# Performance work log

Hardware: AMD Instinct MI355X
Metric: run time of the kernel (lower is better)

The kernel has to match this reference:

```python
import jax, jax.numpy as jnp
import numpy as np

B, S, D, H = 2, 2048, 1024, 16
HD = D // H  # head dim = 64


def setup_inputs() -> dict:
    key = jax.random.key(0)
    ks = jax.random.split(key, 12)
    s = 1.0 / np.sqrt(D)
    return {
        "query": jax.random.normal(ks[0], (B, S, D), jnp.float32),
        "key": jax.random.normal(ks[1], (B, S, D), jnp.float32),
        "value": jax.random.normal(ks[2], (B, S, D), jnp.float32),
        "mask": jax.random.randint(ks[3], (B, S, S), 0, 2, jnp.int32),
        "wq_kernel": jax.random.normal(ks[4], (D, D), jnp.float32) * s,
        "wq_bias": jnp.zeros((D,), jnp.float32),
        "wk_kernel": jax.random.normal(ks[5], (D, D), jnp.float32) * s,
        "wk_bias": jnp.zeros((D,), jnp.float32),
        "wv_kernel": jax.random.normal(ks[6], (D, D), jnp.float32) * s,
        "wv_bias": jnp.zeros((D,), jnp.float32),
        "wo_kernel": jax.random.normal(ks[7], (D, D), jnp.float32) * s,
        "wo_bias": jnp.zeros((D,), jnp.float32),
    }


def reference(query, key, value, mask,
              wq_kernel, wq_bias, wk_kernel, wk_bias,
              wv_kernel, wv_bias, wo_kernel, wo_bias):
    b = query.shape[0]
    # Dense projections, then split heads: [B,S,D] -> [B,H,S,HD]
    def split_heads(x):
        return x.reshape(b, -1, H, HD).transpose(0, 2, 1, 3)

    q = split_heads(query @ wq_kernel + wq_bias)
    k = split_heads(key @ wk_kernel + wk_bias)
    v = split_heads(value @ wv_kernel + wv_bias)

    scores = jnp.einsum('bhqd,bhkd->bhqk', q, k) / jnp.sqrt(jnp.float32(HD))
    m = mask[:, None, :, :]  # [B,1,S,S] broadcast over heads
    scores = jnp.where(m == 0, jnp.float32(-1e9), scores)
    attn = jax.nn.softmax(scores, axis=-1)
    out = jnp.einsum('bhqk,bhkd->bhqd', attn, v)
    out = out.transpose(0, 2, 1, 3).reshape(b, -1, D)  # [B,S,D]
    return out @ wo_kernel + wo_bias
```

## Files before the change

### kernel.cpp

```cpp
#include <hip/hip_runtime.h>
#include <hip/hip_bf16.h>

typedef __attribute__((ext_vector_type(8))) short bf16x8;
typedef __attribute__((ext_vector_type(4))) float f32x4;
typedef __attribute__((ext_vector_type(2))) unsigned int u32x2;
typedef unsigned long long u64;
typedef unsigned short u16;
typedef unsigned int u32;

#define LOG2E 1.44269504088896340736f

__device__ __forceinline__ u16 f2bf(float f) {
  u32 u = __builtin_bit_cast(u32, f);
  u32 r = u + 0x7FFFu + ((u >> 16) & 1u);
  return (u16)(r >> 16);
}

__device__ __forceinline__ u32 cvt_pk_bf16(float lo, float hi) {
  u32 r;
  asm("v_cvt_pk_bf16_f32 %0, %1, %2" : "=v"(r) : "v"(lo), "v"(hi));
  return r;
}

__device__ __forceinline__ float fexp2(float x) {
#if __has_builtin(__builtin_amdgcn_exp2f)
  return __builtin_amdgcn_exp2f(x);
#else
  return exp2f(x);
#endif
}

__device__ __forceinline__ void gload16(const u16* g, u16* l) {
  __builtin_amdgcn_global_load_lds(
      (const __attribute__((address_space(1))) u32*)g,
      (__attribute__((address_space(3))) u32*)l, 16, 0, 0);
}

__global__ __launch_bounds__(256) void cvt_bf16(const float* __restrict__ q,
                                                const float* __restrict__ k,
                                                const float* __restrict__ v,
                                                u16* __restrict__ out) {
  const float* src = (blockIdx.y == 0) ? q : (blockIdx.y == 1) ? k : v;
  u16* dst = out + (size_t)blockIdx.y * 4194304;
  size_t i = ((size_t)blockIdx.x * 256 + threadIdx.x) * 8;
  float4 a = *(const float4*)(src + i);
  float4 b = *(const float4*)(src + i + 4);
  u16 t[8] = {f2bf(a.x), f2bf(a.y), f2bf(a.z), f2bf(a.w),
              f2bf(b.x), f2bf(b.y), f2bf(b.z), f2bf(b.w)};
  *(bf16x8*)(dst + i) = *(bf16x8*)t;
}

__global__ __launch_bounds__(256) void mask_bits(const int* __restrict__ mask,
                                                 u64* __restrict__ out) {
  const int nwords = 2 * 2048 * 32;
  int gw = (blockIdx.x * 256 + threadIdx.x) >> 6;
  int lane = threadIdx.x & 63;
  int nw = (gridDim.x * 256) >> 6;
  for (int w = gw; w < nwords; w += nw) {
    int m = mask[(size_t)w * 64 + lane];
    u64 bits = __ballot(m != 0);
    if (lane == 0) out[w] = bits;
  }
}

__global__ __launch_bounds__(256) void wtrans(const float* __restrict__ W0,
                                              const float* __restrict__ W1,
                                              const float* __restrict__ W2,
                                              const float* __restrict__ W3,
                                              u16* __restrict__ WtBase) {
  const float* W = (blockIdx.z == 0) ? W0 : (blockIdx.z == 1) ? W1
                    : (blockIdx.z == 2) ? W2 : W3;
  u16* T = WtBase + (size_t)blockIdx.z * 1048576;
  __shared__ float tile[32][33];
  int k0 = blockIdx.y * 32, n0 = blockIdx.x * 32;
  int tx = threadIdx.x, ty = threadIdx.y;
#pragma unroll
  for (int i = 0; i < 4; i++)
    tile[ty + i * 8][tx] = W[(size_t)(k0 + ty + i * 8) * 1024 + n0 + tx];
  __syncthreads();
#pragma unroll
  for (int i = 0; i < 4; i++)
    T[(size_t)(n0 + ty + i * 8) * 1024 + k0 + tx] = f2bf(tile[tx][ty + i * 8]);
}

__global__ __launch_bounds__(256) void vtrans(const u16* __restrict__ Vb,
                                              u16* __restrict__ Vt) {
  __shared__ u16 t[64][72];
  int bh = blockIdx.y, k0 = blockIdx.x * 64;
  const u16* src = Vb + (size_t)bh * 2048 * 64;
  u16* dst = Vt + (size_t)bh * 64 * 2048;
  int tid = threadIdx.x;
  int r = tid >> 2, c = (tid & 3) * 16;
  *(bf16x8*)&t[r][c] = *(const bf16x8*)(src + (size_t)(k0 + r) * 64 + c);
  *(bf16x8*)&t[r][c + 8] = *(const bf16x8*)(src + (size_t)(k0 + r) * 64 + c + 8);
  __syncthreads();
  int d = tid >> 2, kb = (tid & 3) * 16;
  u16 tmp[16];
#pragma unroll
  for (int i = 0; i < 16; i++) tmp[i] = t[kb + i][d];
  *(bf16x8*)(dst + (size_t)d * 2048 + k0 + kb) = *(bf16x8*)&tmp[0];
  *(bf16x8*)(dst + (size_t)d * 2048 + k0 + kb + 8) = *(bf16x8*)&tmp[8];
}

__global__ __launch_bounds__(256, 2) void gemm_qkv(
    const u16* __restrict__ Ab, const float* __restrict__ bq,
    const float* __restrict__ bk, const float* __restrict__ bv,
    const u16* __restrict__ WtBase, u16* __restrict__ OutBase) {
  constexpr int K = 1024;
  __shared__ alignas(16) u16 As[128][32];
  __shared__ alignas(16) u16 Bs[128][32];
  const int z = blockIdx.z;
  const u16* A = Ab + (size_t)z * 4194304;
  const float* bias = (z == 0) ? bq : (z == 1) ? bk : bv;
  const u16* Bt = WtBase + (size_t)z * 1048576;
  u16* Ob = OutBase + (size_t)z * 4194304;
  const float scale = (z == 0) ? 0.125f * LOG2E : 1.0f;

  const int tid = threadIdx.x;
  const int lane = tid & 63, wave = tid >> 6;
  const int wr = wave >> 1, wc = wave & 1;
  const int m0 = blockIdx.y * 128, n0 = blockIdx.x * 128;
  const int fr = lane & 15, fq = lane >> 4;

  const int srow = lane >> 2, scol = (lane & 3) * 8;
  const u16* Agp = A + (size_t)(m0 + wave * 32 + srow) * K + scol;
  const u16* Bgp = Bt + (size_t)(n0 + wave * 32 + srow) * K + scol;
  u16* As0 = &As[wave * 32][0];
  u16* As1 = &As[wave * 32 + 16][0];
  u16* Bs0 = &Bs[wave * 32][0];
  u16* Bs1 = &Bs[wave * 32 + 16][0];

  f32x4 acc[4][4];
#pragma unroll
  for (int i = 0; i < 4; i++)
#pragma unroll
    for (int j = 0; j < 4; j++) acc[i][j] = (f32x4){0.f, 0.f, 0.f, 0.f};

  for (int k0 = 0; k0 < K; k0 += 32) {
    gload16(Agp + k0, As0);
    gload16(Agp + k0 + 16 * K, As1);
    gload16(Bgp + k0, Bs0);
    gload16(Bgp + k0 + 16 * K, Bs1);
    __syncthreads();
    bf16x8 af[4], bfv[4];
#pragma unroll
    for (int i = 0; i < 4; i++) {
      af[i] = *(const bf16x8*)&As[wr * 64 + i * 16 + fr][fq * 8];
      bfv[i] = *(const bf16x8*)&Bs[wc * 64 + i * 16 + fr][fq * 8];
    }
#pragma unroll
    for (int i = 0; i < 4; i++)
#pragma unroll
      for (int j = 0; j < 4; j++)
        acc[i][j] = __builtin_amdgcn_mfma_f32_16x16x32_bf16(af[i], bfv[j],
                                                            acc[i][j], 0, 0, 0);
    __syncthreads();
  }
#pragma unroll
  for (int j = 0; j < 4; j++) {
    int col = n0 + wc * 64 + j * 16 + fr;
    float bcol = bias[col];
    int hh = col >> 6, hd = col & 63;
#pragma unroll
    for (int i = 0; i < 4; i++) {
#pragma unroll
      for (int r = 0; r < 4; r++) {
        int row = m0 + wr * 64 + i * 16 + fq * 4 + r;
        int bb = row >> 11, ss = row & 2047;
        float val = (acc[i][j][r] + bcol) * scale;
        Ob[(((size_t)bb * 16 + hh) * 2048 + ss) * 64 + hd] = f2bf(val);
      }
    }
  }
}

__global__ __launch_bounds__(256, 2) void gemm_out(const u16* __restrict__ A,
                                                   const u16* __restrict__ Bt,
                                                   const float* __restrict__ bias,
                                                   float* __restrict__ Out) {
  constexpr int K = 1024;
  __shared__ alignas(16) u16 As[64][32];
  __shared__ alignas(16) u16 Bs[128][32];
  const int tid = threadIdx.x;
  const int lane = tid & 63, wave = tid >> 6;
  const int wr = wave >> 1, wc = wave & 1;
  const int m0 = blockIdx.y * 64, n0 = blockIdx.x * 128;
  const int fr = lane & 15, fq = lane >> 4;

  const int srow = lane >> 2, scol = (lane & 3) * 8;
  const u16* Agp = A + (size_t)(m0 + wave * 16 + srow) * K + scol;
  const u16* Bgp = Bt + (size_t)(n0 + wave * 32 + srow) * K + scol;
  u16* As0 = &As[wave * 16][0];
  u16* Bs0 = &Bs[wave * 32][0];
  u16* Bs1 = &Bs[wave * 32 + 16][0];

  f32x4 acc[2][4];
#pragma unroll
  for (int i = 0; i < 2; i++)
#pragma unroll
    for (int j = 0; j < 4; j++) acc[i][j] = (f32x4){0.f, 0.f, 0.f, 0.f};

  for (int k0 = 0; k0 < K; k0 += 32) {
    gload16(Agp + k0, As0);
    gload16(Bgp + k0, Bs0);
    gload16(Bgp + k0 + 16 * K, Bs1);
    __syncthreads();
    bf16x8 af[2], bfv[4];
#pragma unroll
    for (int i = 0; i < 2; i++)
      af[i] = *(const bf16x8*)&As[wr * 32 + i * 16 + fr][fq * 8];
#pragma unroll
    for (int j = 0; j < 4; j++)
      bfv[j] = *(const bf16x8*)&Bs[wc * 64 + j * 16 + fr][fq * 8];
#pragma unroll
    for (int i = 0; i < 2; i++)
#pragma unroll
      for (int j = 0; j < 4; j++)
        acc[i][j] = __builtin_amdgcn_mfma_f32_16x16x32_bf16(af[i], bfv[j],
                                                            acc[i][j], 0, 0, 0);
    __syncthreads();
  }
#pragma unroll
  for (int j = 0; j < 4; j++) {
    int col = n0 + wc * 64 + j * 16 + fr;
    float bcol = bias[col];
#pragma unroll
    for (int i = 0; i < 2; i++) {
#pragma unroll
      for (int r = 0; r < 4; r++) {
        int row = m0 + wr * 32 + i * 16 + fq * 4 + r;
        Out[(size_t)row * 1024 + col] = acc[i][j][r] + bcol;
      }
    }
  }
}

__global__ __launch_bounds__(256, 4) void attn(const u16* __restrict__ Qb,
                                               const u16* __restrict__ Kb,
                                               const u16* __restrict__ Vtb,
                                               const u64* __restrict__ mbits,
                                               u16* __restrict__ AO) {
  int fid = blockIdx.x + (blockIdx.y << 5) + ((int)blockIdx.z << 9);
  int nfid = ((fid & 7) << 7) + (fid >> 3);
  const int qt = nfid & 31, h = (nfid >> 5) & 15, b = nfid >> 9;
  const int bh = b * 16 + h, q0 = qt * 64;
  const u16* Qh = Qb + (size_t)bh * 2048 * 64;
  const u16* Kh = Kb + (size_t)bh * 2048 * 64;
  const u16* Vh = Vtb + (size_t)bh * 64 * 2048;

  __shared__ u16 Kbuf[2][64][64];
  __shared__ u16 Vbuf[2][64][64];
  __shared__ u16 Ps[4][16][64];

  const int tid = threadIdx.x, lane = tid & 63, wave = tid >> 6;
  const int fr = lane & 15, fq = lane >> 4;
  const int l3 = lane >> 3, l7 = lane & 7;
  const int srcoff = ((l7 ^ l3) * 8);
  const int sw = fr & 7;
  const int sw4 = sw << 4;

  {
    const u16* qsrc = Qh + (size_t)(q0 + wave * 16 + l3) * 64 + srcoff;
    gload16(qsrc, &Vbuf[1][wave * 16][0]);
    gload16(qsrc + 8 * 64, &Vbuf[1][wave * 16 + 8][0]);
    const u16* ksrc = Kh + (size_t)(wave * 16 + l3) * 64 + srcoff;
    gload16(ksrc, &Kbuf[0][wave * 16][0]);
    gload16(ksrc + 8 * 64, &Kbuf[0][wave * 16 + 8][0]);
    const u16* vsrc = Vh + (size_t)(wave * 16 + l3) * 2048 + srcoff;
    gload16(vsrc, &Vbuf[0][wave * 16][0]);
    gload16(vsrc + 8 * 2048, &Vbuf[0][wave * 16 + 8][0]);
  }
  __syncthreads();
  bf16x8 qf0 = *(const bf16x8*)&Vbuf[1][wave * 16 + fr][(fq ^ sw) * 8];
  bf16x8 qf1 = *(const bf16x8*)&Vbuf[1][wave * 16 + fr][((4 + fq) ^ sw) * 8];
  __syncthreads();

  f32x4 accO[4];
#pragma unroll
  for (int i = 0; i < 4; i++) accO[i] = (f32x4){0.f, 0.f, 0.f, 0.f};
  float mrun = -1e30f, lrun = 0.f;

  const u64* mrow = mbits + ((size_t)b * 2048 + q0 + wave * 16 + fr) * 32;
  const u16* kpre = Kh + (size_t)(64 + wave * 16 + l3) * 64 + srcoff;
  const u16* vpre = Vh + (size_t)(wave * 16 + l3) * 2048 + 64 + srcoff;
  u64 wcur = mrow[0];

  for (int kt = 0; kt < 32; kt++) {
    const int cur = kt & 1, nxt = cur ^ 1;
    u64 wnxt = 0;
    if (kt < 31) {
      gload16(kpre, &Kbuf[nxt][wave * 16][0]);
      gload16(kpre + 8 * 64, &Kbuf[nxt][wave * 16 + 8][0]);
      gload16(vpre, &Vbuf[nxt][wave * 16][0]);
      gload16(vpre + 8 * 2048, &Vbuf[nxt][wave * 16 + 8][0]);
      kpre += 64 * 64;
      vpre += 64;
      wnxt = mrow[kt + 1];
    }
    u32 wlo = (u32)wcur, whi = (u32)(wcur >> 32);

    f32x4 sf[4];
    __builtin_amdgcn_s_setprio(1);
#pragma unroll
    for (int f = 0; f < 4; f++) {
      u32 half = (f & 2) ? whi : wlo;
      u32 nib = (half >> ((f & 1) * 16 + fq * 4)) & 0xFu;
      f32x4 zz;
      zz[0] = (nib & 1u) ? 0.f : -3e38f;
      zz[1] = (nib & 2u) ? 0.f : -3e38f;
      zz[2] = (nib & 4u) ? 0.f : -3e38f;
      zz[3] = (nib & 8u) ? 0.f : -3e38f;
      bf16x8 kf0 = *(const bf16x8*)&Kbuf[cur][f * 16 + fr][(fq ^ sw) * 8];
      bf16x8 kf1 = *(const bf16x8*)&Kbuf[cur][f * 16 + fr][((4 + fq) ^ sw) * 8];
      zz = __builtin_amdgcn_mfma_f32_16x16x32_bf16(kf0, qf0, zz, 0, 0, 0);
      zz = __builtin_amdgcn_mfma_f32_16x16x32_bf16(kf1, qf1, zz, 0, 0, 0);
      sf[f] = zz;
    }
    __builtin_amdgcn_s_setprio(0);

    float t0 = fmaxf(fmaxf(sf[0][0], sf[0][1]), sf[0][2]);
    float t1 = fmaxf(fmaxf(sf[0][3], sf[1][0]), sf[1][1]);
    float t2 = fmaxf(fmaxf(sf[1][2], sf[1][3]), sf[2][0]);
    float t3 = fmaxf(fmaxf(sf[2][1], sf[2][2]), sf[2][3]);
    float t4 = fmaxf(fmaxf(sf[3][0], sf[3][1]), sf[3][2]);
    float rm = fmaxf(fmaxf(fmaxf(t0, t1), fmaxf(t2, t3)),
                     fmaxf(t4, sf[3][3]));
    rm = fmaxf(rm, __shfl_xor(rm, 16));
    rm = fmaxf(rm, __shfl_xor(rm, 32));
    if (!__all(rm <= mrun + 8.f)) {
      float mnew = fmaxf(mrun, rm);
      float sc = fexp2(mrun - mnew);
      mrun = mnew;
      lrun *= sc;
      float sc0 = __shfl(sc, fq * 4 + 0);
      float sc1 = __shfl(sc, fq * 4 + 1);
      float sc2 = __shfl(sc, fq * 4 + 2);
      float sc3 = __shfl(sc, fq * 4 + 3);
#pragma unroll
      for (int hs = 0; hs < 4; hs++) {
        accO[hs][0] *= sc0;
        accO[hs][1] *= sc1;
        accO[hs][2] *= sc2;
        accO[hs][3] *= sc3;
      }
    }
    float rs = 0.f;
    u32 pk0[4], pk1[4];
#pragma unroll
    for (int f = 0; f < 4; f++) {
      float p0 = fexp2(sf[f][0] - mrun);
      float p1 = fexp2(sf[f][1] - mrun);
      float p2 = fexp2(sf[f][2] - mrun);
      float p3 = fexp2(sf[f][3] - mrun);
      rs += (p0 + p1) + (p2 + p3);
      pk0[f] = cvt_pk_bf16(p0, p1);
      pk1[f] = cvt_pk_bf16(p2, p3);
    }
    rs += __shfl_xor(rs, 16);
    rs += __shfl_xor(rs, 32);
    lrun += rs;
    char* Pw = (char*)&Ps[wave][fr][0];
#pragma unroll
    for (int f = 0; f < 4; f++) {
      int boff = (f * 32 + fq * 8) ^ sw4;
      *(u32x2*)(Pw + boff) = (u32x2){pk0[f], pk1[f]};
    }
    __builtin_amdgcn_s_setprio(1);
#pragma unroll
    for (int ks = 0; ks < 2; ks++) {
      bf16x8 pa = *(const bf16x8*)(Pw + (((ks * 4 + fq) << 4) ^ sw4));
#pragma unroll
      for (int hs = 0; hs < 4; hs++) {
        bf16x8 vf =
            *(const bf16x8*)&Vbuf[cur][hs * 16 + fr][((ks * 4 + fq) ^ sw) * 8];
        accO[hs] =
            __builtin_amdgcn_mfma_f32_16x16x32_bf16(pa, vf, accO[hs], 0, 0, 0);
      }
    }
    __builtin_amdgcn_s_setprio(0);
    wcur = wnxt;
    __syncthreads();
  }
  float lq0 = fmaxf(__shfl(lrun, fq * 4 + 0), 1e-30f);
  float lq1 = fmaxf(__shfl(lrun, fq * 4 + 1), 1e-30f);
  float lq2 = fmaxf(__shfl(lrun, fq * 4 + 2), 1e-30f);
  float lq3 = fmaxf(__shfl(lrun, fq * 4 + 3), 1e-30f);
#pragma unroll
  for (int hs = 0; hs < 4; hs++) {
    int d = hs * 16 + fr;
    size_t base = ((size_t)b * 2048 + q0 + wave * 16) * 1024 + h * 64 + d;
    AO[base + (size_t)(fq * 4 + 0) * 1024] = f2bf(accO[hs][0] / lq0);
    AO[base + (size_t)(fq * 4 + 1) * 1024] = f2bf(accO[hs][1] / lq1);
    AO[base + (size_t)(fq * 4 + 2) * 1024] = f2bf(accO[hs][2] / lq2);
    AO[base + (size_t)(fq * 4 + 3) * 1024] = f2bf(accO[hs][3] / lq3);
  }
}

extern "C" void kernel_launch(void* const* d_in, const int* in_sizes, int n_in,
                              void* d_out, int out_size, void* d_ws,
                              size_t ws_size, hipStream_t stream) {
  const float* q = (const float*)d_in[0];
  const float* k = (const float*)d_in[1];
  const float* v = (const float*)d_in[2];
  const int* mask = (const int*)d_in[3];
  const float* wq = (const float*)d_in[4];
  const float* bq = (const float*)d_in[5];
  const float* wk = (const float*)d_in[6];
  const float* bk = (const float*)d_in[7];
  const float* wv = (const float*)d_in[8];
  const float* bv = (const float*)d_in[9];
  const float* wo = (const float*)d_in[10];
  const float* bo = (const float*)d_in[11];

  char* ws = (char*)d_ws;
  u16* Wt = (u16*)(ws);
  u16* Qb = (u16*)(ws + (size_t)(8u << 20));
  u16* Kb = (u16*)(ws + (size_t)(16u << 20));
  u16* Vb = (u16*)(ws + (size_t)(24u << 20));
  u16* Ab = (u16*)(ws + (size_t)(32u << 20));
  u16* AO = (u16*)(ws + (size_t)(32u << 20));
  u64* mb = (u64*)(ws + (size_t)(40u << 20));
  u16* Vt = (u16*)(ws + (size_t)(41u << 20));

  cvt_bf16<<<dim3(2048, 3), dim3(256), 0, stream>>>(q, k, v, Ab);
  wtrans<<<dim3(32, 32, 4), dim3(32, 8), 0, stream>>>(wq, wk, wv, wo, Wt);
  gemm_qkv<<<dim3(8, 32, 3), dim3(256), 0, stream>>>(Ab, bq, bk, bv, Wt, Qb);
  mask_bits<<<dim3(2048), dim3(256), 0, stream>>>(mask, mb);
  vtrans<<<dim3(32, 32), dim3(256), 0, stream>>>(Vb, Vt);
  attn<<<dim3(32, 16, 2), dim3(256), 0, stream>>>(Qb, Kb, Vt, mb, AO);
  gemm_out<<<dim3(8, 64, 1), dim3(256), 0, stream>>>(AO, Wt + 3 * 1048576, bo,
                                                     (float*)d_out);
}
```

Measured before the change: 159.3 us.

## Rewrite attention with 32x32 MFMA tiles, 128-query blocks and register P

The attention kernel now gives each wave 32 queries instead of 16, so a block covers 128 queries, and it uses 32x32x16 bf16 MFMA for both QK^T and PV. The probability tile is passed from the score accumulators to the PV operand in registers with v_permlane32_swap, so the per-wave LDS round trip for P is gone. Output is staged through LDS so each row is written to global memory with 16-byte stores. This halves K/V reloads per query and cuts shuffles, but it raises register use (launch bounds drop to 2 blocks) and halves the grid to 512 blocks.

```diff
diff --git a/kernel.cpp b/kernel.cpp
--- a/kernel.cpp
+++ b/kernel.cpp
@@ -3,7 +3,9 @@
 
 typedef __attribute__((ext_vector_type(8))) short bf16x8;
 typedef __attribute__((ext_vector_type(4))) float f32x4;
+typedef __attribute__((ext_vector_type(16))) float f32x16;
 typedef __attribute__((ext_vector_type(2))) unsigned int u32x2;
+typedef __attribute__((ext_vector_type(4))) unsigned int u32x4;
 typedef unsigned long long u64;
 typedef unsigned short u16;
 typedef unsigned int u32;
@@ -20,6 +22,10 @@
   u32 r;
   asm("v_cvt_pk_bf16_f32 %0, %1, %2" : "=v"(r) : "v"(lo), "v"(hi));
   return r;
+}
+
+__device__ __forceinline__ void swap32(u32& a, u32& b) {
+  asm("v_permlane32_swap_b32 %0, %1" : "+v"(a), "+v"(b));
 }
 
 __device__ __forceinline__ float fexp2(float x) {
@@ -235,164 +241,188 @@
   }
 }
 
-__global__ __launch_bounds__(256, 4) void attn(const u16* __restrict__ Qb,
+__global__ __launch_bounds__(256, 2) void attn(const u16* __restrict__ Qb,
                                                const u16* __restrict__ Kb,
                                                const u16* __restrict__ Vtb,
                                                const u64* __restrict__ mbits,
                                                u16* __restrict__ AO) {
-  int fid = blockIdx.x + (blockIdx.y << 5) + ((int)blockIdx.z << 9);
-  int nfid = ((fid & 7) << 7) + (fid >> 3);
-  const int qt = nfid & 31, h = (nfid >> 5) & 15, b = nfid >> 9;
-  const int bh = b * 16 + h, q0 = qt * 64;
+  const int fid = blockIdx.x;
+  const int nfid = ((fid & 7) << 6) + (fid >> 3);
+  const int qt = nfid & 15, bh = nfid >> 4;
+  const int h = bh & 15, b = bh >> 4;
+  const int q0 = qt * 128;
   const u16* Qh = Qb + (size_t)bh * 2048 * 64;
   const u16* Kh = Kb + (size_t)bh * 2048 * 64;
   const u16* Vh = Vtb + (size_t)bh * 64 * 2048;
 
-  __shared__ u16 Kbuf[2][64][64];
-  __shared__ u16 Vbuf[2][64][64];
-  __shared__ u16 Ps[4][16][64];
+  __shared__ u16 smem[18432];
+  u16* KB = smem;
+  u16* VB = smem + 8192;
 
   const int tid = threadIdx.x, lane = tid & 63, wave = tid >> 6;
-  const int fr = lane & 15, fq = lane >> 4;
-  const int l3 = lane >> 3, l7 = lane & 7;
-  const int srcoff = ((l7 ^ l3) * 8);
-  const int sw = fr & 7;
-  const int sw4 = sw << 4;
+  const int ql = lane & 31, hi = lane >> 5;
+  const int l3 = (lane >> 3) & 7, l7 = lane & 7;
+  const int srcoff = (l7 ^ l3) * 8;
+  const int swz = ql & 7;
 
   {
-    const u16* qsrc = Qh + (size_t)(q0 + wave * 16 + l3) * 64 + srcoff;
-    gload16(qsrc, &Vbuf[1][wave * 16][0]);
-    gload16(qsrc + 8 * 64, &Vbuf[1][wave * 16 + 8][0]);
     const u16* ksrc = Kh + (size_t)(wave * 16 + l3) * 64 + srcoff;
-    gload16(ksrc, &Kbuf[0][wave * 16][0]);
-    gload16(ksrc + 8 * 64, &Kbuf[0][wave * 16 + 8][0]);
+    gload16(ksrc, KB + wave * 16 * 64);
+    gload16(ksrc + 8 * 64, KB + (wave * 16 + 8) * 64);
     const u16* vsrc = Vh + (size_t)(wave * 16 + l3) * 2048 + srcoff;
-    gload16(vsrc, &Vbuf[0][wave * 16][0]);
-    gload16(vsrc + 8 * 2048, &Vbuf[0][wave * 16 + 8][0]);
-  }
-  __syncthreads();
-  bf16x8 qf0 = *(const bf16x8*)&Vbuf[1][wave * 16 + fr][(fq ^ sw) * 8];
-  bf16x8 qf1 = *(const bf16x8*)&Vbuf[1][wave * 16 + fr][((4 + fq) ^ sw) * 8];
-  __syncthreads();
-
-  f32x4 accO[4];
-#pragma unroll
-  for (int i = 0; i < 4; i++) accO[i] = (f32x4){0.f, 0.f, 0.f, 0.f};
+    gload16(vsrc, VB + wave * 16 * 64);
+    gload16(vsrc + 8 * 2048, VB + (wave * 16 + 8) * 64);
+  }
+  const int q = q0 + wave * 32 + ql;
+  bf16x8 qf[4];
+  {
+    const u16* qp = Qh + (size_t)q * 64 + hi * 8;
+#pragma unroll
+    for (int kd = 0; kd < 4; kd++) qf[kd] = *(const bf16x8*)(qp + kd * 16);
+  }
+  f32x16 accO0, accO1;
+#pragma unroll
+  for (int i = 0; i < 16; i++) {
+    accO0[i] = 0.f;
+    accO1[i] = 0.f;
+  }
   float mrun = -1e30f, lrun = 0.f;
-
-  const u64* mrow = mbits + ((size_t)b * 2048 + q0 + wave * 16 + fr) * 32;
+  const u64* mrow = mbits + ((size_t)b * 2048 + q) * 32;
   const u16* kpre = Kh + (size_t)(64 + wave * 16 + l3) * 64 + srcoff;
   const u16* vpre = Vh + (size_t)(wave * 16 + l3) * 2048 + 64 + srcoff;
   u64 wcur = mrow[0];
+  __syncthreads();
 
   for (int kt = 0; kt < 32; kt++) {
-    const int cur = kt & 1, nxt = cur ^ 1;
+    const int cur = kt & 1;
+    const u16* KBc = KB + cur * 4096;
+    const u16* VBc = VB + cur * 4096;
+    u16* KBn = KB + (cur ^ 1) * 4096;
+    u16* VBn = VB + (cur ^ 1) * 4096;
     u64 wnxt = 0;
     if (kt < 31) {
-      gload16(kpre, &Kbuf[nxt][wave * 16][0]);
-      gload16(kpre + 8 * 64, &Kbuf[nxt][wave * 16 + 8][0]);
-      gload16(vpre, &Vbuf[nxt][wave * 16][0]);
-      gload16(vpre + 8 * 2048, &Vbuf[nxt][wave * 16 + 8][0]);
+      gload16(kpre, KBn + wave * 16 * 64);
+      gload16(kpre + 8 * 64, KBn + (wave * 16 + 8) * 64);
+      gload16(vpre, VBn + wave * 16 * 64);
+      gload16(vpre + 8 * 2048, VBn + (wave * 16 + 8) * 64);
       kpre += 64 * 64;
       vpre += 64;
       wnxt = mrow[kt + 1];
     }
-    u32 wlo = (u32)wcur, whi = (u32)(wcur >> 32);
-
-    f32x4 sf[4];
+    const u32 wlo = (u32)wcur, wh = (u32)(wcur >> 32);
+
+    f32x16 sf0, sf1;
+#pragma unroll
+    for (int g = 0; g < 4; g++) {
+      u32 nib0 = (wlo >> (8 * g + 4 * hi)) & 0xFu;
+      u32 nib1 = (wh >> (8 * g + 4 * hi)) & 0xFu;
+      sf0[4 * g + 0] = (nib0 & 1u) ? 0.f : -3e38f;
+      sf0[4 * g + 1] = (nib0 & 2u) ? 0.f : -3e38f;
+      sf0[4 * g + 2] = (nib0 & 4u) ? 0.f : -3e38f;
+      sf0[4 * g + 3] = (nib0 & 8u) ? 0.f : -3e38f;
+      sf1[4 * g + 0] = (nib1 & 1u) ? 0.f : -3e38f;
+      sf1[4 * g + 1] = (nib1 & 2u) ? 0.f : -3e38f;
+      sf1[4 * g + 2] = (nib1 & 4u) ? 0.f : -3e38f;
+      sf1[4 * g + 3] = (nib1 & 8u) ? 0.f : -3e38f;
+    }
     __builtin_amdgcn_s_setprio(1);
 #pragma unroll
-    for (int f = 0; f < 4; f++) {
-      u32 half = (f & 2) ? whi : wlo;
-      u32 nib = (half >> ((f & 1) * 16 + fq * 4)) & 0xFu;
-      f32x4 zz;
-      zz[0] = (nib & 1u) ? 0.f : -3e38f;
-      zz[1] = (nib & 2u) ? 0.f : -3e38f;
-      zz[2] = (nib & 4u) ? 0.f : -3e38f;
-      zz[3] = (nib & 8u) ? 0.f : -3e38f;
-      bf16x8 kf0 = *(const bf16x8*)&Kbuf[cur][f * 16 + fr][(fq ^ sw) * 8];
-      bf16x8 kf1 = *(const bf16x8*)&Kbuf[cur][f * 16 + fr][((4 + fq) ^ sw) * 8];
-      zz = __builtin_amdgcn_mfma_f32_16x16x32_bf16(kf0, qf0, zz, 0, 0, 0);
-      zz = __builtin_amdgcn_mfma_f32_16x16x32_bf16(kf1, qf1, zz, 0, 0, 0);
-      sf[f] = zz;
+    for (int kd = 0; kd < 4; kd++) {
+      bf16x8 kf0 = *(const bf16x8*)&KBc[ql * 64 + ((2 * kd + hi) ^ swz) * 8];
+      bf16x8 kf1 =
+          *(const bf16x8*)&KBc[(32 + ql) * 64 + ((2 * kd + hi) ^ swz) * 8];
+      sf0 = __builtin_amdgcn_mfma_f32_32x32x16_bf16(kf0, qf[kd], sf0, 0, 0, 0);
+      sf1 = __builtin_amdgcn_mfma_f32_32x32x16_bf16(kf1, qf[kd], sf1, 0, 0, 0);
     }
     __builtin_amdgcn_s_setprio(0);
 
-    float t0 = fmaxf(fmaxf(sf[0][0], sf[0][1]), sf[0][2]);
-    float t1 = fmaxf(fmaxf(sf[0][3], sf[1][0]), sf[1][1]);
-    float t2 = fmaxf(fmaxf(sf[1][2], sf[1][3]), sf[2][0]);
-    float t3 = fmaxf(fmaxf(sf[2][1], sf[2][2]), sf[2][3]);
-    float t4 = fmaxf(fmaxf(sf[3][0], sf[3][1]), sf[3][2]);
-    float rm = fmaxf(fmaxf(fmaxf(t0, t1), fmaxf(t2, t3)),
-                     fmaxf(t4, sf[3][3]));
-    rm = fmaxf(rm, __shfl_xor(rm, 16));
+    float rm = fmaxf(sf0[0], sf0[1]);
+#pragma unroll
+    for (int i = 2; i < 16; i += 2) rm = fmaxf(rm, fmaxf(sf0[i], sf0[i + 1]));
+#pragma unroll
+    for (int i = 0; i < 16; i += 2) rm = fmaxf(rm, fmaxf(sf1[i], sf1[i + 1]));
     rm = fmaxf(rm, __shfl_xor(rm, 32));
     if (!__all(rm <= mrun + 8.f)) {
       float mnew = fmaxf(mrun, rm);
       float sc = fexp2(mrun - mnew);
       mrun = mnew;
       lrun *= sc;
-      float sc0 = __shfl(sc, fq * 4 + 0);
-      float sc1 = __shfl(sc, fq * 4 + 1);
-      float sc2 = __shfl(sc, fq * 4 + 2);
-      float sc3 = __shfl(sc, fq * 4 + 3);
-#pragma unroll
-      for (int hs = 0; hs < 4; hs++) {
-        accO[hs][0] *= sc0;
-        accO[hs][1] *= sc1;
-        accO[hs][2] *= sc2;
-        accO[hs][3] *= sc3;
+#pragma unroll
+      for (int i = 0; i < 16; i++) {
+        accO0[i] *= sc;
+        accO1[i] *= sc;
       }
     }
     float rs = 0.f;
-    u32 pk0[4], pk1[4];
-#pragma unroll
-    for (int f = 0; f < 4; f++) {
-      float p0 = fexp2(sf[f][0] - mrun);
-      float p1 = fexp2(sf[f][1] - mrun);
-      float p2 = fexp2(sf[f][2] - mrun);
-      float p3 = fexp2(sf[f][3] - mrun);
-      rs += (p0 + p1) + (p2 + p3);
-      pk0[f] = cvt_pk_bf16(p0, p1);
-      pk1[f] = cvt_pk_bf16(p2, p3);
-    }
-    rs += __shfl_xor(rs, 16);
+#pragma unroll
+    for (int i = 0; i < 16; i++) {
+      sf0[i] = fexp2(sf0[i] - mrun);
+      rs += sf0[i];
+    }
+#pragma unroll
+    for (int i = 0; i < 16; i++) {
+      sf1[i] = fexp2(sf1[i] - mrun);
+      rs += sf1[i];
+    }
     rs += __shfl_xor(rs, 32);
     lrun += rs;
-    char* Pw = (char*)&Ps[wave][fr][0];
-#pragma unroll
-    for (int f = 0; f < 4; f++) {
-      int boff = (f * 32 + fq * 8) ^ sw4;
-      *(u32x2*)(Pw + boff) = (u32x2){pk0[f], pk1[f]};
-    }
+
+    bf16x8 pf[4];
+#pragma unroll
+    for (int g = 0; g < 4; g++) {
+      int r0 = (g & 1) * 8;
+      u32 A, A2, Bv, B2;
+      if (g < 2) {
+        A = cvt_pk_bf16(sf0[r0 + 0], sf0[r0 + 1]);
+        A2 = cvt_pk_bf16(sf0[r0 + 2], sf0[r0 + 3]);
+        Bv = cvt_pk_bf16(sf0[r0 + 4], sf0[r0 + 5]);
+        B2 = cvt_pk_bf16(sf0[r0 + 6], sf0[r0 + 7]);
+      } else {
+        A = cvt_pk_bf16(sf1[r0 + 0], sf1[r0 + 1]);
+        A2 = cvt_pk_bf16(sf1[r0 + 2], sf1[r0 + 3]);
+        Bv = cvt_pk_bf16(sf1[r0 + 4], sf1[r0 + 5]);
+        B2 = cvt_pk_bf16(sf1[r0 + 6], sf1[r0 + 7]);
+      }
+      swap32(A, Bv);
+      swap32(A2, B2);
+      u32x4 t = (u32x4){A, A2, Bv, B2};
+      pf[g] = __builtin_bit_cast(bf16x8, t);
+    }
+
     __builtin_amdgcn_s_setprio(1);
 #pragma unroll
-    for (int ks = 0; ks < 2; ks++) {
-      bf16x8 pa = *(const bf16x8*)(Pw + (((ks * 4 + fq) << 4) ^ sw4));
-#pragma unroll
-      for (int hs = 0; hs < 4; hs++) {
-        bf16x8 vf =
-            *(const bf16x8*)&Vbuf[cur][hs * 16 + fr][((ks * 4 + fq) ^ sw) * 8];
-        accO[hs] =
-            __builtin_amdgcn_mfma_f32_16x16x32_bf16(pa, vf, accO[hs], 0, 0, 0);
-      }
+    for (int ks = 0; ks < 4; ks++) {
+      bf16x8 vf0 = *(const bf16x8*)&VBc[ql * 64 + ((2 * ks + hi) ^ swz) * 8];
+      bf16x8 vf1 =
+          *(const bf16x8*)&VBc[(32 + ql) * 64 + ((2 * ks + hi) ^ swz) * 8];
+      accO0 = __builtin_amdgcn_mfma_f32_32x32x16_bf16(vf0, pf[ks], accO0, 0, 0, 0);
+      accO1 = __builtin_amdgcn_mfma_f32_32x32x16_bf16(vf1, pf[ks], accO1, 0, 0, 0);
     }
     __builtin_amdgcn_s_setprio(0);
     wcur = wnxt;
     __syncthreads();
   }
-  float lq0 = fmaxf(__shfl(lrun, fq * 4 + 0), 1e-30f);
-  float lq1 = fmaxf(__shfl(lrun, fq * 4 + 1), 1e-30f);
-  float lq2 = fmaxf(__shfl(lrun, fq * 4 + 2), 1e-30f);
-  float lq3 = fmaxf(__shfl(lrun, fq * 4 + 3), 1e-30f);
-#pragma unroll
-  for (int hs = 0; hs < 4; hs++) {
-    int d = hs * 16 + fr;
-    size_t base = ((size_t)b * 2048 + q0 + wave * 16) * 1024 + h * 64 + d;
-    AO[base + (size_t)(fq * 4 + 0) * 1024] = f2bf(accO[hs][0] / lq0);
-    AO[base + (size_t)(fq * 4 + 1) * 1024] = f2bf(accO[hs][1] / lq1);
-    AO[base + (size_t)(fq * 4 + 2) * 1024] = f2bf(accO[hs][2] / lq2);
-    AO[base + (size_t)(fq * 4 + 3) * 1024] = f2bf(accO[hs][3] / lq3);
+
+  float inv = 1.f / fmaxf(lrun, 1e-30f);
+  __syncthreads();
+  u16* OT = smem;
+  const int orow = wave * 32 + ql;
+#pragma unroll
+  for (int s = 0; s < 8; s++) {
+    int d0 = (2 * s & 3) + 8 * (s >> 1) + 4 * hi;
+    u32 p0 = cvt_pk_bf16(accO0[2 * s] * inv, accO0[2 * s + 1] * inv);
+    u32 p1 = cvt_pk_bf16(accO1[2 * s] * inv, accO1[2 * s + 1] * inv);
+    *(u32*)&OT[orow * 72 + d0] = p0;
+    *(u32*)&OT[orow * 72 + 32 + d0] = p1;
+  }
+  __syncthreads();
+  {
+    int rq = tid >> 1, c0 = (tid & 1) * 32;
+    const u16* src = &OT[rq * 72 + c0];
+    u16* dst = AO + ((size_t)(b * 2048 + q0 + rq)) * 1024 + h * 64 + c0;
+#pragma unroll
+    for (int i = 0; i < 4; i++)
+      *(bf16x8*)(dst + i * 8) = *(const bf16x8*)(src + i * 8);
   }
 }
 
@@ -427,7 +457,7 @@
   gemm_qkv<<<dim3(8, 32, 3), dim3(256), 0, stream>>>(Ab, bq, bk, bv, Wt, Qb);
   mask_bits<<<dim3(2048), dim3(256), 0, stream>>>(mask, mb);
   vtrans<<<dim3(32, 32), dim3(256), 0, stream>>>(Vb, Vt);
-  attn<<<dim3(32, 16, 2), dim3(256), 0, stream>>>(Qb, Kb, Vt, mb, AO);
+  attn<<<dim3(512), dim3(256), 0, stream>>>(Qb, Kb, Vt, mb, AO);
   gemm_out<<<dim3(8, 64, 1), dim3(256), 0, stream>>>(AO, Wt + 3 * 1048576, bo,
                                                      (float*)d_out);
 }
```

Result: faster. 152.6 us (-4.2%).
